# Optimization experiments

Hardware: AMD Instinct MI355X
Metric: run time of the kernel (lower is better)

The kernel has to match this reference:

```python
import math
import jax, jax.numpy as jnp
import numpy as np

L, H, D, FF, V, S = 12, 12, 768, 3072, 32000, 1024
HD = D // H
EPS = 1e-5
B, T = 2, 1024


def layernorm(x, w, b):
    mu = jnp.mean(x, axis=-1, keepdims=True)
    var = jnp.mean(jnp.square(x - mu), axis=-1, keepdims=True)
    return (x - mu) * jax.lax.rsqrt(var + EPS) * w + b


def setup_inputs() -> dict:
    key = jax.random.key(0)
    ks = jax.random.split(key, 12)
    std = 0.02
    std_res = 0.02 / math.sqrt(2 * L)  # out_proj / down_proj scaled init
    return {
        "input_ids": jax.random.randint(ks[0], (B, T), 0, V),
        "tok_emb": jax.random.normal(ks[1], (V, D), jnp.float32) * std,
        "pos_emb": jax.random.normal(ks[2], (S, D), jnp.float32) * std,
        "ln1_w": jnp.ones((L, D), jnp.float32),
        "ln1_b": jnp.zeros((L, D), jnp.float32),
        "qkv_w": jax.random.normal(ks[3], (L, 3 * D, D), jnp.float32) * std,
        "out_w": jax.random.normal(ks[4], (L, D, D), jnp.float32) * std_res,
        "ln2_w": jnp.ones((L, D), jnp.float32),
        "ln2_b": jnp.zeros((L, D), jnp.float32),
        "up_w": jax.random.normal(ks[5], (L, FF, D), jnp.float32) * std,
        "down_w": jax.random.normal(ks[6], (L, D, FF), jnp.float32) * std_res,
        "lnf_w": jnp.ones((D,), jnp.float32),
        "lnf_b": jnp.zeros((D,), jnp.float32),
    }


def reference(input_ids, tok_emb, pos_emb, ln1_w, ln1_b, qkv_w, out_w,
              ln2_w, ln2_b, up_w, down_w, lnf_w, lnf_b):
    b, t = input_ids.shape
    x = tok_emb[input_ids] + pos_emb[:t]  # (B,T,D); dropout = eval no-op
    causal = jnp.tril(jnp.ones((t, t), bool))  # (T,T)
    scale = 1.0 / math.sqrt(HD)

    def block(x, p):
        l1w, l1b, qkvw, ow, l2w, l2b, uw, dw = p
        h = layernorm(x, l1w, l1b)
        qkv = h @ qkvw.T  # (B,T,3D)
        q, k, v = jnp.split(qkv, 3, axis=-1)
        q = q.reshape(b, t, H, HD)
        k = k.reshape(b, t, H, HD)
        v = v.reshape(b, t, H, HD)
        scores = jnp.einsum('bihd,bjhd->bhij', q, k) * scale
        scores = jnp.where(causal, scores, -jnp.inf)
        probs = jax.nn.softmax(scores, axis=-1)  # attn_dropout = eval no-op
        o = jnp.einsum('bhij,bjhd->bihd', probs, v).reshape(b, t, D)
        x = x + o @ ow.T
        h2 = layernorm(x, l2w, l2b)
        x = x + jax.nn.gelu(h2 @ uw.T, approximate=False) @ dw.T
        return x, None

    x, _ = jax.lax.scan(block, x, (ln1_w, ln1_b, qkv_w, out_w, ln2_w, ln2_b, up_w, down_w))
    x = layernorm(x, lnf_w, lnf_b)
    logits = x @ tok_emb.T  # tied lm_head
    return logits
```

## Files before the change

### kernel.cpp

```cpp
#include <hip/hip_runtime.h>
#include <hip/hip_bf16.h>
#include <math.h>

#define L_  12
#define H_  12
#define D_  768
#define FF_ 3072
#define V_  32000
#define T_  1024
#define B_  2
#define BT_ (B_*T_)

typedef unsigned short ushort_t;
typedef unsigned int   uint_t;
typedef __bf16 bf16x8 __attribute__((ext_vector_type(8)));
typedef float  f32x4  __attribute__((ext_vector_type(4)));

__device__ __forceinline__ uint_t f2bf1(float f) {
    uint_t u = __builtin_bit_cast(uint_t, f);
    return (u + 0x7FFFu + ((u >> 16) & 1u)) >> 16;
}
__device__ __forceinline__ uint_t f2bf2(float lo, float hi) {
    return f2bf1(lo) | (f2bf1(hi) << 16);
}

__device__ __forceinline__ void gl_lds16(const ushort_t* g, ushort_t* l) {
    __builtin_amdgcn_global_load_lds(
        (const __attribute__((address_space(1))) uint_t*)g,
        (__attribute__((address_space(3))) uint_t*)l, 16, 0, 0);
}

__global__ __launch_bounds__(256) void cast_bf16(const float* __restrict__ in,
                                                 ushort_t* __restrict__ out, int n8)
{
    for (int i = blockIdx.x * 256 + threadIdx.x; i < n8; i += gridDim.x * 256) {
        const float4* p = (const float4*)(in + (size_t)i * 8);
        float4 a = p[0], b = p[1];
        *(uint4*)(out + (size_t)i * 8) =
            make_uint4(f2bf2(a.x,a.y), f2bf2(a.z,a.w), f2bf2(b.x,b.y), f2bf2(b.z,b.w));
    }
}

__global__ __launch_bounds__(256) void cast_layer(const float* __restrict__ q,
    const float* __restrict__ o, const float* __restrict__ u, const float* __restrict__ d,
    ushort_t* __restrict__ out)
{
    const int N0 = 3*D_*D_/8, N1 = N0 + D_*D_/8, N2 = N1 + FF_*D_/8, N3 = N2 + D_*FF_/8;
    for (int i = blockIdx.x * 256 + threadIdx.x; i < N3; i += gridDim.x * 256) {
        const float* src;
        if      (i < N0) src = q + (size_t)i * 8;
        else if (i < N1) src = o + (size_t)(i - N0) * 8;
        else if (i < N2) src = u + (size_t)(i - N1) * 8;
        else             src = d + (size_t)(i - N2) * 8;
        const float4* p = (const float4*)src;
        float4 a = p[0], b = p[1];
        *(uint4*)(out + (size_t)i * 8) =
            make_uint4(f2bf2(a.x,a.y), f2bf2(a.z,a.w), f2bf2(b.x,b.y), f2bf2(b.z,b.w));
    }
}

#define EPI_F32   0
#define EPI_BF16  1
#define EPI_GELU  2
#define EPI_PART  3
#define EPI_QKV   4

template <int EPI, int BM, int KS>
__global__ __launch_bounds__(256) void gemm_bt(
    const ushort_t* __restrict__ A, const ushort_t* __restrict__ W,
    const float* R, void* Cv, ushort_t* __restrict__ Vt, int N, int K, int Kc)
{
    constexpr int MI = BM / 32;
    constexpr int AH = BM * 32;
    constexpr int BH = 128 * 32;
    __shared__ ushort_t As[2 * AH];
    __shared__ ushort_t Bs[2 * BH];

    const int tid  = threadIdx.x;
    const int w    = tid >> 6;
    const int lane = tid & 63;

    const int nwg = gridDim.x;
    int swz = (blockIdx.x & 7) * (nwg >> 3) + (blockIdx.x >> 3);
    constexpr int MT = 2048 / BM;
    const int mt = swz & (MT - 1);
    int rest     = swz / MT;
    const int ks = rest & (KS - 1);
    const int nt = rest / KS;
    const int m0 = mt * BM, n0 = nt * 128;
    const int kb = ks * Kc;

    const int srow = lane >> 2;
    const int scol = ((lane & 3) ^ ((srow >> 1) & 3)) * 8;
    const ushort_t* gA = A + (size_t)(m0 + w * (BM / 4) + srow) * K + scol;
    const ushort_t* gW = W + (size_t)(n0 + w * 32 + srow) * K + scol;
    const size_t row16 = (size_t)16 * K;

    const int lr = lane & 15;
    const int lg = lane >> 4;
    const int wm = (w >> 1) * (BM / 2);
    const int wn = (w & 1) * 64;

    f32x4 acc[MI][4] = {};

    auto stage = [&](int buf, int k0) {
        ushort_t* lA = As + buf * AH + w * (BM / 4) * 32;
        ushort_t* lB = Bs + buf * BH + w * 1024;
        #pragma unroll
        for (int i = 0; i < BM / 64; ++i)
            gl_lds16(gA + k0 + i * row16, lA + i * 512);
        #pragma unroll
        for (int i = 0; i < 2; ++i)
            gl_lds16(gW + k0 + i * row16, lB + i * 512);
    };

    stage(0, kb);
    __syncthreads();
    int cur = 0;
    for (int k0 = kb; k0 < kb + Kc; k0 += 32) {
        if (k0 + 32 < kb + Kc) stage(cur ^ 1, k0 + 32);
        const ushort_t* Ab = As + cur * AH;
        const ushort_t* Bb = Bs + cur * BH;
        __builtin_amdgcn_s_setprio(1);
        {
            bf16x8 av[MI], bv[4];
            #pragma unroll
            for (int i = 0; i < MI; ++i) {
                int rr = wm + i * 16 + lr;
                int ch = lg ^ ((rr >> 1) & 3);
                av[i] = *(const bf16x8*)&Ab[rr * 32 + ch * 8];
            }
            #pragma unroll
            for (int j = 0; j < 4; ++j) {
                int rr = wn + j * 16 + lr;
                int ch = lg ^ ((rr >> 1) & 3);
                bv[j] = *(const bf16x8*)&Bb[rr * 32 + ch * 8];
            }
            #pragma unroll
            for (int i = 0; i < MI; ++i)
                #pragma unroll
                for (int j = 0; j < 4; ++j)
                    acc[i][j] = __builtin_amdgcn_mfma_f32_16x16x32_bf16(av[i], bv[j], acc[i][j], 0, 0, 0);
        }
        __builtin_amdgcn_s_setprio(0);
        __syncthreads();
        cur ^= 1;
    }

    float*    Cf = (float*)Cv;
    ushort_t* Cb = (ushort_t*)Cv;
    float*    Pp = (EPI == EPI_PART) ? (const_cast<float*>(R) + (size_t)ks * BT_ * D_) : nullptr;
    const int rbase = lg * 4;
    #pragma unroll
    for (int i = 0; i < MI; ++i) {
        #pragma unroll
        for (int j = 0; j < 4; ++j) {
            const int row0 = m0 + wm + i * 16 + rbase;
            const int col  = n0 + wn + j * 16 + lr;
            if (EPI == EPI_QKV) {
                if (col < 1536) {
                    #pragma unroll
                    for (int r = 0; r < 4; ++r)
                        Cb[(size_t)(row0 + r) * 2304 + col] = (ushort_t)f2bf1(acc[i][j][r]);
                } else {
                    const int hh = (col - 1536) >> 6, dd = (col - 1536) & 63;
                    const int bb = row0 >> 10,        tt = row0 & 1023;
                    uint2 pk;
                    pk.x = f2bf2(acc[i][j][0], acc[i][j][1]);
                    pk.y = f2bf2(acc[i][j][2], acc[i][j][3]);
                    *(uint2*)&Vt[(((size_t)bb * H_ + hh) * 64 + dd) * T_ + tt] = pk;
                }
            } else {
                #pragma unroll
                for (int r = 0; r < 4; ++r) {
                    size_t idx = (size_t)(row0 + r) * N + col;
                    float v = acc[i][j][r];
                    if (EPI == EPI_F32)  Cf[idx] = v;
                    if (EPI == EPI_BF16) Cb[idx] = (ushort_t)f2bf1(v);
                    if (EPI == EPI_GELU) Cb[idx] = (ushort_t)f2bf1(0.5f * v * (1.0f + erff(v * 0.70710678118654752f)));
                    if (EPI == EPI_PART) Pp[idx] = v;
                }
            }
        }
    }
}

__global__ __launch_bounds__(64) void attn_mfma(const ushort_t* __restrict__ qkv,
    const ushort_t* __restrict__ vt, ushort_t* __restrict__ o)
{
    __shared__ ushort_t Ps[16 * 136];

    int swz = (blockIdx.x & 7) * 192 + (blockIdx.x >> 3);
    const int bh  = swz >> 6;
    const int qtl = 63 - (swz & 63);
    const int b   = bh / H_;
    const int h   = bh % H_;
    const int lane = threadIdx.x;
    const int l15  = lane & 15;
    const int lg   = lane >> 4;
    const int qbase = qtl * 16;
    const int qlast = qbase + 15;

    const ushort_t* qp = qkv + ((size_t)(b * T_) + qbase + l15) * 2304 + h * 64 + lg * 8;
    bf16x8 qf0 = *(const bf16x8*)qp;
    bf16x8 qf1 = *(const bf16x8*)(qp + 32);

    f32x4 od[4] = {};
    float mr[4] = {-INFINITY, -INFINITY, -INFINITY, -INFINITY};
    float lr[4] = {0.f, 0.f, 0.f, 0.f};

    const ushort_t* kbase = qkv + (size_t)(b * T_) * 2304 + 768 + h * 64;
    const ushort_t* vbase = vt + (size_t)bh * 64 * T_;
    const float SC = 0.18033688011112042f;

    for (int j0 = 0; j0 <= qlast; j0 += 128) {
        f32x4 s[8];
        __builtin_amdgcn_s_setprio(1);
        #pragma unroll
        for (int n = 0; n < 8; ++n) {
            if (j0 + 16 * n <= qlast) {
                const ushort_t* kr = kbase + (size_t)(j0 + 16 * n + l15) * 2304 + lg * 8;
                bf16x8 kf0 = *(const bf16x8*)kr;
                bf16x8 kf1 = *(const bf16x8*)(kr + 32);
                f32x4 a = {};
                a = __builtin_amdgcn_mfma_f32_16x16x32_bf16(qf0, kf0, a, 0, 0, 0);
                a = __builtin_amdgcn_mfma_f32_16x16x32_bf16(qf1, kf1, a, 0, 0, 0);
                s[n] = a;
            } else {
                s[n] = f32x4{-INFINITY, -INFINITY, -INFINITY, -INFINITY};
            }
        }
        __builtin_amdgcn_s_setprio(0);

        #pragma unroll
        for (int n = 0; n < 8; ++n) {
            #pragma unroll
            for (int r = 0; r < 4; ++r) {
                float v = s[n][r] * SC;
                int jg = j0 + 16 * n + l15;
                int qg = qbase + lg * 4 + r;
                if (jg > qg) v = -INFINITY;
                s[n][r] = v;
            }
        }

        float al[4];
        #pragma unroll
        for (int r = 0; r < 4; ++r) {
            float tm = fmaxf(fmaxf(fmaxf(s[0][r], s[1][r]), fmaxf(s[2][r], s[3][r])),
                             fmaxf(fmaxf(s[4][r], s[5][r]), fmaxf(s[6][r], s[7][r])));
            tm = fmaxf(tm, __shfl_xor(tm, 1, 64));
            tm = fmaxf(tm, __shfl_xor(tm, 2, 64));
            tm = fmaxf(tm, __shfl_xor(tm, 4, 64));
            tm = fmaxf(tm, __shfl_xor(tm, 8, 64));
            float mn = fmaxf(mr[r], tm);
            al[r] = exp2f(mr[r] - mn);
            mr[r] = mn;
        }
        #pragma unroll
        for (int n = 0; n < 8; ++n)
            #pragma unroll
            for (int r = 0; r < 4; ++r)
                s[n][r] = exp2f(s[n][r] - mr[r]);
        #pragma unroll
        for (int r = 0; r < 4; ++r) {
            float ps = (s[0][r] + s[1][r]) + (s[2][r] + s[3][r]);
            ps += (s[4][r] + s[5][r]) + (s[6][r] + s[7][r]);
            ps += __shfl_xor(ps, 1, 64);
            ps += __shfl_xor(ps, 2, 64);
            ps += __shfl_xor(ps, 4, 64);
            ps += __shfl_xor(ps, 8, 64);
            lr[r] = lr[r] * al[r] + ps;
        }
        #pragma unroll
        for (int n = 0; n < 4; ++n)
            #pragma unroll
            for (int r = 0; r < 4; ++r)
                od[n][r] *= al[r];

        #pragma unroll
        for (int n = 0; n < 8; ++n)
            #pragma unroll
            for (int r = 0; r < 4; ++r)
                Ps[(lg * 4 + r) * 136 + 16 * n + l15] = (ushort_t)f2bf1(s[n][r]);

        __builtin_amdgcn_s_setprio(1);
        #pragma unroll
        for (int kc = 0; kc < 4; ++kc) {
            if (j0 + kc * 32 <= qlast) {
                bf16x8 pa = *(const bf16x8*)&Ps[l15 * 136 + kc * 32 + lg * 8];
                #pragma unroll
                for (int nn = 0; nn < 4; ++nn) {
                    bf16x8 vf = *(const bf16x8*)&vbase[(size_t)(16 * nn + l15) * T_ + j0 + kc * 32 + lg * 8];
                    od[nn] = __builtin_amdgcn_mfma_f32_16x16x32_bf16(pa, vf, od[nn], 0, 0, 0);
                }
            }
        }
        __builtin_amdgcn_s_setprio(0);
    }

    #pragma unroll
    for (int r = 0; r < 4; ++r) {
        float inv = 1.0f / lr[r];
        int row = qbase + lg * 4 + r;
        ushort_t* op = o + ((size_t)(b * T_ + row)) * 768 + h * 64 + l15;
        #pragma unroll
        for (int nn = 0; nn < 4; ++nn)
            op[16 * nn] = (ushort_t)f2bf1(od[nn][r] * inv);
    }
}

__device__ __forceinline__ void ln_body(float v0, float v1, float v2,
    const float* __restrict__ w, const float* __restrict__ bia,
    ushort_t* __restrict__ orow, int tid)
{
    float s  = v0 + v1 + v2;
    float s2 = v0 * v0 + v1 * v1 + v2 * v2;
    #pragma unroll
    for (int off = 32; off > 0; off >>= 1) {
        s  += __shfl_down(s,  off, 64);
        s2 += __shfl_down(s2, off, 64);
    }
    __shared__ float sh[8];
    const int wave = tid >> 6;
    if ((tid & 63) == 0) { sh[wave] = s; sh[4 + wave] = s2; }
    __syncthreads();
    float S  = sh[0] + sh[1] + sh[2] + sh[3];
    float S2 = sh[4] + sh[5] + sh[6] + sh[7];
    float mean = S * (1.f / 768.f);
    float var  = S2 * (1.f / 768.f) - mean * mean;
    float inv  = rsqrtf(var + 1e-5f);
    orow[tid]       = (ushort_t)f2bf1((v0 - mean) * inv * w[tid]       + bia[tid]);
    orow[tid + 256] = (ushort_t)f2bf1((v1 - mean) * inv * w[tid + 256] + bia[tid + 256]);
    orow[tid + 512] = (ushort_t)f2bf1((v2 - mean) * inv * w[tid + 512] + bia[tid + 512]);
}

__global__ __launch_bounds__(256) void ln_red4(float* __restrict__ x,
    const float* __restrict__ P, const float* __restrict__ w,
    const float* __restrict__ bia, ushort_t* __restrict__ out)
{
    const int row = blockIdx.x;
    const int tid = threadIdx.x;
    const size_t base = (size_t)row * 768;
    const size_t st = (size_t)BT_ * D_;
    float v0 = x[base + tid];
    float v1 = x[base + tid + 256];
    float v2 = x[base + tid + 512];
    #pragma unroll
    for (int p = 0; p < 4; ++p) {
        v0 += P[p * st + base + tid];
        v1 += P[p * st + base + tid + 256];
        v2 += P[p * st + base + tid + 512];
    }
    x[base + tid]       = v0;
    x[base + tid + 256] = v1;
    x[base + tid + 512] = v2;
    ln_body(v0, v1, v2, w, bia, out + base, tid);
}

__global__ __launch_bounds__(256) void embed_ln(const int* __restrict__ ids,
    const float* __restrict__ tok, const float* __restrict__ pos,
    const float* __restrict__ w, const float* __restrict__ bia,
    float* __restrict__ x, ushort_t* __restrict__ out)
{
    const int bt = blockIdx.x;
    const int t  = bt % T_;
    const int id = ids[bt];
    const int tid = threadIdx.x;
    const float* tr = tok + (size_t)id * 768;
    const float* pr = pos + (size_t)t * 768;
    const size_t base = (size_t)bt * 768;
    float v0 = tr[tid]       + pr[tid];
    float v1 = tr[tid + 256] + pr[tid + 256];
    float v2 = tr[tid + 512] + pr[tid + 512];
    x[base + tid]       = v0;
    x[base + tid + 256] = v1;
    x[base + tid + 512] = v2;
    ln_body(v0, v1, v2, w, bia, out + base, tid);
}

extern "C" void kernel_launch(void* const* d_in, const int* in_sizes, int n_in,
                              void* d_out, int out_size, void* d_ws, size_t ws_size,
                              hipStream_t stream)
{
    const int*   ids   = (const int*)  d_in[0];
    const float* tok   = (const float*)d_in[1];
    const float* pos   = (const float*)d_in[2];
    const float* ln1w  = (const float*)d_in[3];
    const float* ln1b  = (const float*)d_in[4];
    const float* qkvw  = (const float*)d_in[5];
    const float* outw  = (const float*)d_in[6];
    const float* ln2w  = (const float*)d_in[7];
    const float* ln2b  = (const float*)d_in[8];
    const float* upw   = (const float*)d_in[9];
    const float* downw = (const float*)d_in[10];
    const float* lnfw  = (const float*)d_in[11];
    const float* lnfb  = (const float*)d_in[12];
    float* out = (float*)d_out;

    char* ws = (char*)d_ws;
    ushort_t* h    = (ushort_t*)ws;
    float*    x    = (float*)   (ws + 3145728);
    ushort_t* qkv  = (ushort_t*)(ws + 9437184);
    ushort_t* o    = qkv  + (size_t)BT_ * 3 * D_;
    ushort_t* vt   = o    + (size_t)BT_ * D_;
    ushort_t* ffh  = vt   + (size_t)B_ * H_ * 64 * T_;
    ushort_t* layerW = (ushort_t*)(ws + 50331648);
    ushort_t* tokW   = (ushort_t*)(ws + 67108864);
    float*    P4     = (float*)(ws + 117440512);

    ushort_t* qkvwB  = layerW;
    ushort_t* outwB  = qkvwB + (size_t)3 * D_ * D_;
    ushort_t* upwB   = outwB + (size_t)D_ * D_;
    ushort_t* downwB = upwB  + (size_t)FF_ * D_;

    for (int l = 0; l < L_; ++l) {
        cast_layer<<<1024, 256, 0, stream>>>(
            qkvw  + (size_t)l * 3 * D_ * D_,
            outw  + (size_t)l * D_ * D_,
            upw   + (size_t)l * FF_ * D_,
            downw + (size_t)l * D_ * FF_, layerW);

        if (l == 0)
            embed_ln<<<BT_, 256, 0, stream>>>(ids, tok, pos, ln1w, ln1b, x, h);
        else
            ln_red4<<<BT_, 256, 0, stream>>>(x, P4, ln1w + l * D_, ln1b + l * D_, h);

        gemm_bt<EPI_QKV, 64, 1><<<32 * (3 * D_ / 128), 256, 0, stream>>>(
            h, qkvwB, nullptr, qkv, vt, 3 * D_, D_, D_);

        attn_mfma<<<B_ * H_ * (T_ / 16), 64, 0, stream>>>(qkv, vt, o);

        gemm_bt<EPI_PART, 64, 4><<<32 * (D_ / 128) * 4, 256, 0, stream>>>(
            o, outwB, P4, nullptr, nullptr, D_, D_, D_ / 4);

        ln_red4<<<BT_, 256, 0, stream>>>(x, P4, ln2w + l * D_, ln2b + l * D_, h);

        gemm_bt<EPI_GELU, 64, 1><<<32 * (FF_ / 128), 256, 0, stream>>>(
            h, upwB, nullptr, ffh, nullptr, FF_, D_, D_);

        gemm_bt<EPI_PART, 64, 4><<<32 * (D_ / 128) * 4, 256, 0, stream>>>(
            ffh, downwB, P4, nullptr, nullptr, D_, FF_, FF_ / 4);
    }

    ln_red4<<<BT_, 256, 0, stream>>>(x, P4, lnfw, lnfb, h);

    cast_bf16<<<2048, 256, 0, stream>>>(tok, tokW, V_ * D_ / 8);
    gemm_bt<EPI_F32, 128, 1><<<16 * (V_ / 128), 256, 0, stream>>>(
        h, tokW, nullptr, out, nullptr, V_, D_, D_);
}
```

Measured before the change: 1.985 ms.

## Add 256x256-tile double-buffered MFMA GEMM for the tied LM head

Adds a dedicated GEMM kernel for the final logits projection (2048x32000x768). It uses 256x256 tiles with 512 threads, a double-buffered LDS pipeline fed by direct global-to-LDS loads with an XOR swizzle, and raised wave priority around the MFMA block. The aim is more data reuse per tile and better overlap of loads with compute than the previous 128-wide tile kernel. The cost is 128 KB of LDS per block and a large accumulator register footprint, which may limit occupancy or cause spills.

```diff
diff --git a/kernel.cpp b/kernel.cpp
--- a/kernel.cpp
+++ b/kernel.cpp
@@ -185,6 +185,94 @@
     }
 }
 
+__global__ __launch_bounds__(512, 2) void gemm256(
+    const ushort_t* __restrict__ A, const ushort_t* __restrict__ W,
+    float* __restrict__ C, int N, int K)
+{
+    __shared__ ushort_t Ls[2][2][256 * 64];
+
+    const int tid  = threadIdx.x;
+    const int w    = tid >> 6;
+    const int lane = tid & 63;
+
+    const int nwg = gridDim.x;
+    int swz = (blockIdx.x & 7) * (nwg >> 3) + (blockIdx.x >> 3);
+    const int mt = swz & 7;
+    const int nt = swz >> 3;
+    const int m0 = mt * 256, n0 = nt * 256;
+
+    const int trow = tid >> 3;
+    const int tchk = (tid & 7) ^ (trow & 7);
+    const ushort_t* gA = A + (size_t)(m0 + trow) * K + tchk * 8;
+    const ushort_t* gW = W + (size_t)(n0 + trow) * K + tchk * 8;
+
+    const int lr = lane & 15;
+    const int lg = lane >> 4;
+    const int wm = (w >> 2) * 128;
+    const int wn = (w & 3) * 64;
+
+    f32x4 acc[8][4] = {};
+
+    auto stage = [&](int buf, int k0) {
+        #pragma unroll
+        for (int seg = 0; seg < 4; ++seg) {
+            gl_lds16(gA + (size_t)(seg * 64) * K + k0, &Ls[buf][0][seg * 4096 + w * 512]);
+            gl_lds16(gW + (size_t)(seg * 64) * K + k0, &Ls[buf][1][seg * 4096 + w * 512]);
+        }
+    };
+
+    stage(0, 0);
+    __syncthreads();
+    int cur = 0;
+    const int NT = K / 64;
+    for (int t = 0; t < NT; ++t) {
+        if (t + 1 < NT) stage(cur ^ 1, (t + 1) * 64);
+        const ushort_t* Ab = Ls[cur][0];
+        const ushort_t* Bb = Ls[cur][1];
+        bf16x8 bv[4][2];
+        #pragma unroll
+        for (int nf = 0; nf < 4; ++nf) {
+            int rr = wn + nf * 16 + lr;
+            #pragma unroll
+            for (int kk = 0; kk < 2; ++kk) {
+                int ch = (kk * 4 + lg) ^ (rr & 7);
+                bv[nf][kk] = *(const bf16x8*)&Bb[rr * 64 + ch * 8];
+            }
+        }
+        __builtin_amdgcn_s_setprio(1);
+        #pragma unroll
+        for (int mf = 0; mf < 8; ++mf) {
+            int rr = wm + mf * 16 + lr;
+            int ch0 = lg ^ (rr & 7);
+            int ch1 = (4 + lg) ^ (rr & 7);
+            bf16x8 a0 = *(const bf16x8*)&Ab[rr * 64 + ch0 * 8];
+            bf16x8 a1 = *(const bf16x8*)&Ab[rr * 64 + ch1 * 8];
+            #pragma unroll
+            for (int nf = 0; nf < 4; ++nf) {
+                acc[mf][nf] = __builtin_amdgcn_mfma_f32_16x16x32_bf16(a0, bv[nf][0], acc[mf][nf], 0, 0, 0);
+                acc[mf][nf] = __builtin_amdgcn_mfma_f32_16x16x32_bf16(a1, bv[nf][1], acc[mf][nf], 0, 0, 0);
+            }
+        }
+        __builtin_amdgcn_s_setprio(0);
+        __syncthreads();
+        cur ^= 1;
+    }
+
+    const int rbase = lg * 4;
+    #pragma unroll
+    for (int mf = 0; mf < 8; ++mf) {
+        #pragma unroll
+        for (int nf = 0; nf < 4; ++nf) {
+            #pragma unroll
+            for (int r = 0; r < 4; ++r) {
+                int row = m0 + wm + mf * 16 + rbase + r;
+                int col = n0 + wn + nf * 16 + lr;
+                C[(size_t)row * N + col] = acc[mf][nf][r];
+            }
+        }
+    }
+}
+
 __global__ __launch_bounds__(64) void attn_mfma(const ushort_t* __restrict__ qkv,
     const ushort_t* __restrict__ vt, ushort_t* __restrict__ o)
 {
@@ -446,6 +534,5 @@
     ln_red4<<<BT_, 256, 0, stream>>>(x, P4, lnfw, lnfb, h);
 
     cast_bf16<<<2048, 256, 0, stream>>>(tok, tokW, V_ * D_ / 8);
-    gemm_bt<EPI_F32, 128, 1><<<16 * (V_ / 128), 256, 0, stream>>>(
-        h, tokW, nullptr, out, nullptr, V_, D_, D_);
-}
+    gemm256<<<(2048 / 256) * (V_ / 256), 512, 0, stream>>>(h, tokW, out, V_, D_);
+}
```

Result: no change. 1.977 ms (-0.4%).
